# Kernel tuning notes

Hardware: AMD Instinct MI355X
Metric: run time of the kernel (lower is better)

## Reference

```python
import jax, jax.numpy as jnp
import numpy as np

N_FEATURES = 256
HIDDEN_DIM = 256
NUM_HEADS = 8
HEAD_DIM = HIDDEN_DIM // NUM_HEADS
SCALE = HEAD_DIM ** -0.5
H = W = 64


def setup_inputs() -> dict:
    key = jax.random.key(0)
    k1, k2, kq, kk, kv, kp, kb = jax.random.split(key, 7)
    s = 1.0 / np.sqrt(N_FEATURES)
    return {
        "x1": jax.random.normal(k1, (1, N_FEATURES, H, W), dtype=jnp.float32),
        "x2": jax.random.normal(k2, (1, N_FEATURES, H, W), dtype=jnp.float32),
        # 1x1 conv weights reduce to [out_ch, in_ch] matrices
        "Wq": jax.random.uniform(kq, (HIDDEN_DIM, N_FEATURES), jnp.float32, -s, s),
        "Wk": jax.random.uniform(kk, (HIDDEN_DIM, N_FEATURES), jnp.float32, -s, s),
        "Wv": jax.random.uniform(kv, (HIDDEN_DIM, N_FEATURES), jnp.float32, -s, s),
        "Wp": jax.random.uniform(kp, (N_FEATURES, HIDDEN_DIM), jnp.float32, -s, s),
        "bp": jax.random.uniform(kb, (N_FEATURES,), jnp.float32, -s, s),
    }


def reference(x1, x2, Wq, Wk, Wv, Wp, bp):
    B, C, Hh, Ww = x1.shape
    N = Hh * Ww
    # 1x1 convs == channel matmuls; reshape to [B, heads, head_dim, N]
    q = jnp.einsum('oc,bchw->bohw', Wq, x1).reshape(B, NUM_HEADS, HEAD_DIM, N)
    k = jnp.einsum('oc,bchw->bohw', Wk, x2).reshape(B, NUM_HEADS, HEAD_DIM, N)
    v = jnp.einsum('oc,bchw->bohw', Wv, x2).reshape(B, NUM_HEADS, HEAD_DIM, N)
    attn = jnp.einsum('bhcn,bhcm->bhnm', q, k) * SCALE
    attn = jax.nn.softmax(attn, axis=-1)
    fused = jnp.einsum('bhnm,bhcm->bhcn', attn, v)
    fused = fused.reshape(B, HIDDEN_DIM, Hh, Ww)  # requires hidden_dim == C
    out = jnp.einsum('oc,bchw->bohw', Wp, fused) + bp[None, :, None, None]
    return out
```

## Files before the change

### kernel.cpp

```cpp
#include <hip/hip_runtime.h>

#define NPOS 4096
#define NCH  256
#define HD   32
#define KB   128
#define NSPLIT 4
#define SPLIT_KEYS (NPOS / NSPLIT)
#define NSTEP (SPLIT_KEYS / KB)

#define TOFF(o, c) (((((o) >> 4) * 8 + ((c) >> 5)) * 64 + \
                     ((((c) >> 3) & 3) * 16) + ((o) & 15)) * 8 + ((c) & 7))

typedef float f32x4  __attribute__((ext_vector_type(4)));
typedef float f32x16 __attribute__((ext_vector_type(16)));
typedef short s16x8  __attribute__((ext_vector_type(8)));
typedef uint  u32x2  __attribute__((ext_vector_type(2)));
typedef uint  u32x4  __attribute__((ext_vector_type(4)));
typedef int   i32x2  __attribute__((ext_vector_type(2)));

static __device__ __forceinline__ s16x8 load8(const ushort* p) {
    return *(const s16x8*)p;
}
static __device__ __forceinline__ ushort bfbits(float x) {
    __bf16 b = (__bf16)x;
    return __builtin_bit_cast(unsigned short, b);
}
static __device__ __forceinline__ float bfval(ushort u) {
    uint x = (uint)u << 16;
    return __builtin_bit_cast(float, x);
}
static __device__ __forceinline__ uint pk2(float a, float b) {
    return (uint)bfbits(a) | ((uint)bfbits(b) << 16);
}
static __device__ __forceinline__ void plswap(uint& a, uint& b) {
    i32x2 r = __builtin_amdgcn_permlane32_swap((int)a, (int)b, false, false);
    a = (uint)r[0];
    b = (uint)r[1];
}

__global__ __launch_bounds__(256) void convert_kernel(
    const float* __restrict__ x1, const float* __restrict__ x2,
    const float* __restrict__ Wq, const float* __restrict__ Wk,
    const float* __restrict__ Wv, const float* __restrict__ Wp,
    ushort* __restrict__ xt1h, ushort* __restrict__ xt1l,
    ushort* __restrict__ xt2h, ushort* __restrict__ xt2l,
    ushort* __restrict__ wsp, float qscale)
{
    if (blockIdx.z == 2) {
        const int m = blockIdx.y;
        const float* src = m == 0 ? Wq : m == 1 ? Wk : m == 2 ? Wv : Wp;
        const float sc = m == 0 ? qscale : 1.f;
        const int idx = (blockIdx.x * 256 + threadIdx.x) * 4;
        const int o = idx >> 8, c0 = idx & 255;
        f32x4 w = *(const f32x4*)(src + idx);
        w *= sc;
        ushort h[4], l[4];
#pragma unroll
        for (int i = 0; i < 4; ++i) {
            h[i] = bfbits(w[i]);
            l[i] = bfbits(w[i] - bfval(h[i]));
        }
        ushort* H = wsp + m * 2 * 65536;
        const int off = TOFF(o, c0);
        *(u32x2*)(H + off)         = (u32x2){(uint)h[0] | ((uint)h[1] << 16),
                                             (uint)h[2] | ((uint)h[3] << 16)};
        *(u32x2*)(H + 65536 + off) = (u32x2){(uint)l[0] | ((uint)l[1] << 16),
                                             (uint)l[2] | ((uint)l[3] << 16)};
        return;
    }
    __shared__ float tile[64][65];
    const float* X = blockIdx.z ? x2 : x1;
    ushort* Hd = blockIdx.z ? xt2h : xt1h;
    ushort* Ld = blockIdx.z ? xt2l : xt1l;
    const int n0 = blockIdx.x * 64, c0 = blockIdx.y * 64;
    const int tj = threadIdx.x & 63, ti = threadIdx.x >> 6;
#pragma unroll
    for (int r = 0; r < 16; ++r) {
        int i = r * 4 + ti;
        tile[i][tj] = X[(c0 + i) * NPOS + n0 + tj];
    }
    __syncthreads();
#pragma unroll
    for (int r = 0; r < 16; ++r) {
        int i = r * 4 + ti;
        float v = tile[tj][i];
        ushort h = bfbits(v);
        ushort l = bfbits(v - bfval(h));
        const int off = TOFF(n0 + i, c0 + tj);
        Hd[off] = h;
        Ld[off] = l;
    }
}

__global__ __launch_bounds__(256) void gemm_qkv_kernel(
    const ushort* __restrict__ wsp,
    const ushort* __restrict__ x1h, const ushort* __restrict__ x1l,
    const ushort* __restrict__ x2h, const ushort* __restrict__ x2l,
    ushort* __restrict__ qt, ushort* __restrict__ kt, ushort* __restrict__ vt)
{
    const int m  = blockIdx.y >> 2;
    const int ob = blockIdx.y & 3;
    const ushort* Wh = wsp + m * 131072;
    const ushort* Wl = Wh + 65536;
    const ushort* Bh = (m == 0) ? x1h : x2h;
    const ushort* Bl = (m == 0) ? x1l : x2l;

    const int wid = threadIdx.x >> 6, lane = threadIdx.x & 63;
    const int lq = lane & 15, grp = lane >> 4;
    const int o0 = ob * 64 + wid * 16;
    const int n0 = blockIdx.x * 32;
    const int To = o0 >> 4;
    const int Tn = n0 >> 4;

    f32x4 acc[2];
    acc[0] = (f32x4){0.f, 0.f, 0.f, 0.f};
    acc[1] = acc[0];
#pragma unroll
    for (int kc = 0; kc < 8; ++kc) {
        const s16x8 ah = load8(Wh + ((To * 8 + kc) * 64 + lane) * 8);
        const s16x8 al = load8(Wl + ((To * 8 + kc) * 64 + lane) * 8);
#pragma unroll
        for (int nt = 0; nt < 2; ++nt) {
            const s16x8 bh = load8(Bh + (((Tn + nt) * 8 + kc) * 64 + lane) * 8);
            const s16x8 bl = load8(Bl + (((Tn + nt) * 8 + kc) * 64 + lane) * 8);
            acc[nt] = __builtin_amdgcn_mfma_f32_16x16x32_bf16(ah, bh, acc[nt], 0, 0, 0);
            acc[nt] = __builtin_amdgcn_mfma_f32_16x16x32_bf16(ah, bl, acc[nt], 0, 0, 0);
            acc[nt] = __builtin_amdgcn_mfma_f32_16x16x32_bf16(al, bh, acc[nt], 0, 0, 0);
        }
    }
    if (m < 2) {
        ushort* Y = m ? kt : qt;
        const int head = o0 >> 5, d0 = (o0 & 31) + grp * 4;
#pragma unroll
        for (int nt = 0; nt < 2; ++nt) {
            const int n = n0 + nt * 16 + lq;
            *(u32x2*)(Y + head * (NPOS * HD) + n * HD + d0) =
                (u32x2){pk2(acc[nt][0], acc[nt][1]), pk2(acc[nt][2], acc[nt][3])};
        }
    } else {
#pragma unroll
        for (int nt = 0; nt < 2; ++nt) {
            const int n = n0 + nt * 16 + lq;
#pragma unroll
            for (int r = 0; r < 4; ++r)
                vt[(o0 + grp * 4 + r) * NPOS + n] = bfbits(acc[nt][r]);
        }
    }
}

__global__ __launch_bounds__(256) void attn_mfma_kernel(
    const ushort* __restrict__ Qt,
    const ushort* __restrict__ Kt,
    const ushort* __restrict__ Vt,
    ushort* __restrict__ Opb,
    float* __restrict__ Ml)
{
    __shared__ __align__(16) ushort lds[18944];
    const int bid  = blockIdx.x;
    const int s    = bid >> 8;
    const int h    = bid & 7;
    const int qblk = (bid & 255) >> 3;
    const int tid  = threadIdx.x;
    const int wid  = tid >> 6;
    const int lane = tid & 63;
    const int l31  = lane & 31;
    const int hi   = lane >> 5;
    const int q0   = qblk * 128 + wid * 32;
    const int k0   = s * SPLIT_KEYS;
    const int hq   = h * (NPOS * HD);

    s16x8 qf[2];
#pragma unroll
    for (int kh = 0; kh < 2; ++kh)
        qf[kh] = load8(Qt + hq + (q0 + l31) * HD + kh * 16 + hi * 8);

    const int kr0 = tid >> 2, kc0 = tid & 3;
    const ushort* kS = Kt + hq + kr0 * HD + kc0 * 8;
    const int kdst0 = kr0 * 40 + ((kc0 ^ ((kr0 >> 3) & 3)) & 3) * 8;
    const int kdst1 = kdst0 + 64 * 40;

    const int vr0 = tid >> 4, vc0 = tid & 15;
    const ushort* vS = Vt + h * (HD * NPOS) + vr0 * NPOS + vc0 * 8;
    const int vdst0 = vr0 * 136 + ((vc0 ^ ((vr0 >> 3) & 3)) & 15) * 8;
    const int vdst1 = (vr0 + 16) * 136 +
                      ((vc0 ^ (((vr0 + 16) >> 3) & 3)) & 15) * 8;

    const int kx = l31 >> 3;

    f32x16 oacc = {};
    float lacc = 0.f;

    *(s16x8*)(lds + kdst0)         = load8(kS + (size_t)k0 * HD);
    *(s16x8*)(lds + kdst1)         = load8(kS + (size_t)k0 * HD + 64 * HD);
    *(s16x8*)(lds + 10240 + vdst0) = load8(vS + k0);
    *(s16x8*)(lds + 10240 + vdst1) = load8(vS + k0 + 16 * NPOS);
    const int m1 = (NSTEP > 1) ? k0 + KB : k0;
    s16x8 kra = load8(kS + (size_t)m1 * HD);
    s16x8 krb = load8(kS + (size_t)m1 * HD + 64 * HD);
    s16x8 vra = load8(vS + m1);
    s16x8 vrb = load8(vS + m1 + 16 * NPOS);
    __syncthreads();

    for (int step = 0; step < NSTEP; ++step) {
        const int cur = step & 1;
        ushort* const Kb = lds + cur * 5120;
        ushort* const Vb = lds + 10240 + cur * 4352;

        {
            ushort* const Kn = lds + (cur ^ 1) * 5120;
            ushort* const Vn = lds + 10240 + (cur ^ 1) * 4352;
            *(s16x8*)(Kn + kdst0) = kra;
            *(s16x8*)(Kn + kdst1) = krb;
            *(s16x8*)(Vn + vdst0) = vra;
            *(s16x8*)(Vn + vdst1) = vrb;
        }
        const int mn = (step + 2 < NSTEP) ? k0 + (step + 2) * KB : k0;
        kra = load8(kS + (size_t)mn * HD);
        krb = load8(kS + (size_t)mn * HD + 64 * HD);
        vra = load8(vS + mn);
        vrb = load8(vS + mn + 16 * NPOS);

#pragma unroll
        for (int t = 0; t < 4; ++t) {
            const int krow = (t * 32 + l31) * 40;
            const s16x8 kfa = *(const s16x8*)(Kb + krow + ((hi ^ kx) & 3) * 8);
            const s16x8 kfb = *(const s16x8*)(Kb + krow + (((2 + hi) ^ kx) & 3) * 8);
            f32x16 st = {};
            __builtin_amdgcn_s_setprio(1);
            st = __builtin_amdgcn_mfma_f32_32x32x16_bf16(kfa, qf[0], st, 0, 0, 0);
            st = __builtin_amdgcn_mfma_f32_32x32x16_bf16(kfb, qf[1], st, 0, 0, 0);
            __builtin_amdgcn_s_setprio(0);

            const s16x8 vf0 = *(const s16x8*)(Vb + l31 * 136 +
                                              (((t * 4 + hi) ^ kx) & 15) * 8);
            const s16x8 vf1 = *(const s16x8*)(Vb + l31 * 136 +
                                              (((t * 4 + 2 + hi) ^ kx) & 15) * 8);

            uint w[4], w2[4];
            float ls = 0.f;
#pragma unroll
            for (int g = 0; g < 4; ++g) {
                const float p0 = __builtin_amdgcn_exp2f(st[4 * g + 0]);
                const float p1 = __builtin_amdgcn_exp2f(st[4 * g + 1]);
                const float p2 = __builtin_amdgcn_exp2f(st[4 * g + 2]);
                const float p3 = __builtin_amdgcn_exp2f(st[4 * g + 3]);
                ls += (p0 + p1) + (p2 + p3);
                w[g]  = pk2(p0, p1);
                w2[g] = pk2(p2, p3);
            }
            lacc += ls;
            uint a0 = w[0],  c0 = w[1];  plswap(a0, c0);
            uint a1 = w2[0], c1 = w2[1]; plswap(a1, c1);
            const s16x8 pfA = __builtin_bit_cast(s16x8, (u32x4){a0, a1, c0, c1});
            uint b0 = w[2],  d0 = w[3];  plswap(b0, d0);
            uint b1 = w2[2], d1 = w2[3]; plswap(b1, d1);
            const s16x8 pfB = __builtin_bit_cast(s16x8, (u32x4){b0, b1, d0, d1});

            __builtin_amdgcn_s_setprio(1);
            oacc = __builtin_amdgcn_mfma_f32_32x32x16_bf16(vf0, pfA, oacc, 0, 0, 0);
            oacc = __builtin_amdgcn_mfma_f32_32x32x16_bf16(vf1, pfB, oacc, 0, 0, 0);
            __builtin_amdgcn_s_setprio(0);
        }

        __syncthreads();
    }

    {
        uint a = __builtin_bit_cast(uint, lacc), b = a;
        plswap(a, b);
        lacc = __builtin_bit_cast(float, a) + __builtin_bit_cast(float, b);
    }

    const int n = q0 + l31;
    ushort* Ops = Opb + (size_t)s * (NPOS * NCH) + n * NCH + h * HD;
#pragma unroll
    for (int g = 0; g < 4; ++g) {
        *(u32x2*)(Ops + g * 8 + hi * 4) =
            (u32x2){pk2(oacc[4 * g + 0], oacc[4 * g + 1]),
                    pk2(oacc[4 * g + 2], oacc[4 * g + 3])};
    }
    if (lane < 32)
        Ml[(s * 8 + h) * NPOS + n] = lacc;
}

__global__ __launch_bounds__(256) void combine_kernel(
    const ushort* __restrict__ Opb, const float* __restrict__ Ml,
    ushort* __restrict__ FH, ushort* __restrict__ FL)
{
    const int n = blockIdx.x * 4 + (threadIdx.x >> 6);
    const int c = (threadIdx.x & 63) * 4;
    const int h = c >> 5;
    float l = 0.f;
#pragma unroll
    for (int s = 0; s < NSPLIT; ++s)
        l += Ml[(s * 8 + h) * NPOS + n];
    const float inv = 1.f / l;

    float sum[4] = {0.f, 0.f, 0.f, 0.f};
#pragma unroll
    for (int s = 0; s < NSPLIT; ++s) {
        const u32x2 raw = *(const u32x2*)(Opb + (size_t)s * (NPOS * NCH) +
                                          n * NCH + c);
        sum[0] += bfval((ushort)(raw[0] & 0xFFFF));
        sum[1] += bfval((ushort)(raw[0] >> 16));
        sum[2] += bfval((ushort)(raw[1] & 0xFFFF));
        sum[3] += bfval((ushort)(raw[1] >> 16));
    }
    ushort hb[4], lb[4];
#pragma unroll
    for (int i = 0; i < 4; ++i) {
        float f = sum[i] * inv;
        hb[i] = bfbits(f);
        lb[i] = bfbits(f - bfval(hb[i]));
    }
    const int off = TOFF(n, c);
    *(u32x2*)(FH + off) = (u32x2){(uint)hb[0] | ((uint)hb[1] << 16),
                                  (uint)hb[2] | ((uint)hb[3] << 16)};
    *(u32x2*)(FL + off) = (u32x2){(uint)lb[0] | ((uint)lb[1] << 16),
                                  (uint)lb[2] | ((uint)lb[3] << 16)};
}

__global__ __launch_bounds__(256) void gemm_out_kernel(
    const ushort* __restrict__ Wh, const ushort* __restrict__ Wl,
    const ushort* __restrict__ Bh, const ushort* __restrict__ Bl,
    const float* __restrict__ bias, float* __restrict__ Y)
{
    const int wid = threadIdx.x >> 6, lane = threadIdx.x & 63;
    const int lq = lane & 15, grp = lane >> 4;
    const int o0 = blockIdx.y * 64 + wid * 16;
    const int n0 = blockIdx.x * 32;
    const int To = o0 >> 4;
    const int Tn = n0 >> 4;

    f32x4 acc[2];
    acc[0] = (f32x4){0.f, 0.f, 0.f, 0.f};
    acc[1] = acc[0];
#pragma unroll
    for (int kc = 0; kc < 8; ++kc) {
        const s16x8 ah = load8(Wh + ((To * 8 + kc) * 64 + lane) * 8);
        const s16x8 al = load8(Wl + ((To * 8 + kc) * 64 + lane) * 8);
#pragma unroll
        for (int nt = 0; nt < 2; ++nt) {
            const s16x8 bh = load8(Bh + (((Tn + nt) * 8 + kc) * 64 + lane) * 8);
            const s16x8 bl = load8(Bl + (((Tn + nt) * 8 + kc) * 64 + lane) * 8);
            acc[nt] = __builtin_amdgcn_mfma_f32_16x16x32_bf16(ah, bh, acc[nt], 0, 0, 0);
            acc[nt] = __builtin_amdgcn_mfma_f32_16x16x32_bf16(ah, bl, acc[nt], 0, 0, 0);
            acc[nt] = __builtin_amdgcn_mfma_f32_16x16x32_bf16(al, bh, acc[nt], 0, 0, 0);
        }
    }
    const f32x4 b4 = *(const f32x4*)(bias + o0 + grp * 4);
#pragma unroll
    for (int nt = 0; nt < 2; ++nt) {
        const int n = n0 + nt * 16 + lq;
#pragma unroll
        for (int r = 0; r < 4; ++r)
            Y[(o0 + grp * 4 + r) * NPOS + n] = acc[nt][r] + b4[r];
    }
}

extern "C" void kernel_launch(void* const* d_in, const int* in_sizes, int n_in,
                              void* d_out, int out_size, void* d_ws, size_t ws_size,
                              hipStream_t stream) {
    const float* x1 = (const float*)d_in[0];
    const float* x2 = (const float*)d_in[1];
    const float* Wq = (const float*)d_in[2];
    const float* Wk = (const float*)d_in[3];
    const float* Wv = (const float*)d_in[4];
    const float* Wp = (const float*)d_in[5];
    const float* bp = (const float*)d_in[6];
    float* out = (float*)d_out;

    const size_t MB = 1u << 20;
    char* wsc = (char*)d_ws;
    ushort* xt1h = (ushort*)(wsc + 0 * MB);
    ushort* xt1l = (ushort*)(wsc + 2 * MB);
    ushort* xt2h = (ushort*)(wsc + 4 * MB);
    ushort* xt2l = (ushort*)(wsc + 6 * MB);
    ushort* qt   = (ushort*)(wsc + 8 * MB);
    ushort* kt   = (ushort*)(wsc + 10 * MB);
    ushort* vt   = (ushort*)(wsc + 12 * MB);
    ushort* wsp  = (ushort*)(wsc + 14 * MB);
    float*  Ml   = (float*)(wsc + 15 * MB);
    ushort* Opb  = (ushort*)(wsc + 0 * MB);
    ushort* fth  = (ushort*)(wsc + 8 * MB);
    ushort* ftl  = (ushort*)(wsc + 10 * MB);

    const float qscale = (float)(0.17677669529663687 * 1.4426950408889634);

    convert_kernel<<<dim3(64, 4, 3), 256, 0, stream>>>(
        x1, x2, Wq, Wk, Wv, Wp, xt1h, xt1l, xt2h, xt2l, wsp, qscale);

    gemm_qkv_kernel<<<dim3(128, 12), 256, 0, stream>>>(
        wsp, xt1h, xt1l, xt2h, xt2l, qt, kt, vt);

    attn_mfma_kernel<<<1024, 256, 0, stream>>>(qt, kt, vt, Opb, Ml);

    combine_kernel<<<1024, 256, 0, stream>>>(Opb, Ml, fth, ftl);

    ushort* wph = wsp + 393216;
    ushort* wpl = wsp + 458752;
    gemm_out_kernel<<<dim3(128, 4), 256, 0, stream>>>(
        wph, wpl, fth, ftl, bp, out);
}
```

Before: 75.74 us.

## Fuse input conversion into QKV GEMM and combine into output projection

Splits the weight conversion into its own kernel and folds the x1/x2 transpose and bf16 hi/lo split into the QKV GEMM. Each block now stages its 32-column slice of both inputs in LDS and computes all three projections over 128 output rows. It also merges the split-softmax combine step into the output projection, staging the normalized result in LDS so it is never written to global memory. This removes two kernel launches and the global round trips for the converted activations, at the cost of fewer, heavier blocks (256 blocks each) and more registers per thread.

```diff
diff --git a/kernel.cpp b/kernel.cpp
--- a/kernel.cpp
+++ b/kernel.cpp
@@ -38,114 +38,131 @@
     b = (uint)r[1];
 }
 
-__global__ __launch_bounds__(256) void convert_kernel(
-    const float* __restrict__ x1, const float* __restrict__ x2,
+__global__ __launch_bounds__(256) void convert_w_kernel(
     const float* __restrict__ Wq, const float* __restrict__ Wk,
     const float* __restrict__ Wv, const float* __restrict__ Wp,
-    ushort* __restrict__ xt1h, ushort* __restrict__ xt1l,
-    ushort* __restrict__ xt2h, ushort* __restrict__ xt2l,
     ushort* __restrict__ wsp, float qscale)
 {
-    if (blockIdx.z == 2) {
-        const int m = blockIdx.y;
-        const float* src = m == 0 ? Wq : m == 1 ? Wk : m == 2 ? Wv : Wp;
-        const float sc = m == 0 ? qscale : 1.f;
-        const int idx = (blockIdx.x * 256 + threadIdx.x) * 4;
-        const int o = idx >> 8, c0 = idx & 255;
-        f32x4 w = *(const f32x4*)(src + idx);
-        w *= sc;
-        ushort h[4], l[4];
-#pragma unroll
-        for (int i = 0; i < 4; ++i) {
-            h[i] = bfbits(w[i]);
-            l[i] = bfbits(w[i] - bfval(h[i]));
-        }
-        ushort* H = wsp + m * 2 * 65536;
-        const int off = TOFF(o, c0);
-        *(u32x2*)(H + off)         = (u32x2){(uint)h[0] | ((uint)h[1] << 16),
-                                             (uint)h[2] | ((uint)h[3] << 16)};
-        *(u32x2*)(H + 65536 + off) = (u32x2){(uint)l[0] | ((uint)l[1] << 16),
-                                             (uint)l[2] | ((uint)l[3] << 16)};
-        return;
-    }
-    __shared__ float tile[64][65];
-    const float* X = blockIdx.z ? x2 : x1;
-    ushort* Hd = blockIdx.z ? xt2h : xt1h;
-    ushort* Ld = blockIdx.z ? xt2l : xt1l;
-    const int n0 = blockIdx.x * 64, c0 = blockIdx.y * 64;
-    const int tj = threadIdx.x & 63, ti = threadIdx.x >> 6;
-#pragma unroll
-    for (int r = 0; r < 16; ++r) {
-        int i = r * 4 + ti;
-        tile[i][tj] = X[(c0 + i) * NPOS + n0 + tj];
-    }
-    __syncthreads();
-#pragma unroll
-    for (int r = 0; r < 16; ++r) {
-        int i = r * 4 + ti;
-        float v = tile[tj][i];
-        ushort h = bfbits(v);
-        ushort l = bfbits(v - bfval(h));
-        const int off = TOFF(n0 + i, c0 + tj);
-        Hd[off] = h;
-        Ld[off] = l;
-    }
-}
-
-__global__ __launch_bounds__(256) void gemm_qkv_kernel(
+    const int m = blockIdx.y;
+    const float* src = m == 0 ? Wq : m == 1 ? Wk : m == 2 ? Wv : Wp;
+    const float sc = m == 0 ? qscale : 1.f;
+    const int idx = (blockIdx.x * 256 + threadIdx.x) * 4;
+    const int o = idx >> 8, c0 = idx & 255;
+    f32x4 w = *(const f32x4*)(src + idx);
+    w *= sc;
+    ushort h[4], l[4];
+#pragma unroll
+    for (int i = 0; i < 4; ++i) {
+        h[i] = bfbits(w[i]);
+        l[i] = bfbits(w[i] - bfval(h[i]));
+    }
+    ushort* H = wsp + m * 2 * 65536;
+    const int off = TOFF(o, c0);
+    *(u32x2*)(H + off)         = (u32x2){(uint)h[0] | ((uint)h[1] << 16),
+                                         (uint)h[2] | ((uint)h[3] << 16)};
+    *(u32x2*)(H + 65536 + off) = (u32x2){(uint)l[0] | ((uint)l[1] << 16),
+                                         (uint)l[2] | ((uint)l[3] << 16)};
+}
+
+__global__ __launch_bounds__(256) void fused_qkv_kernel(
+    const float* __restrict__ x1, const float* __restrict__ x2,
     const ushort* __restrict__ wsp,
-    const ushort* __restrict__ x1h, const ushort* __restrict__ x1l,
-    const ushort* __restrict__ x2h, const ushort* __restrict__ x2l,
     ushort* __restrict__ qt, ushort* __restrict__ kt, ushort* __restrict__ vt)
 {
-    const int m  = blockIdx.y >> 2;
-    const int ob = blockIdx.y & 3;
-    const ushort* Wh = wsp + m * 131072;
-    const ushort* Wl = Wh + 65536;
-    const ushort* Bh = (m == 0) ? x1h : x2h;
-    const ushort* Bl = (m == 0) ? x1l : x2l;
-
-    const int wid = threadIdx.x >> 6, lane = threadIdx.x & 63;
+    __shared__ __align__(16) ushort lds[32768];
+    const int tid   = threadIdx.x;
+    const int n0    = blockIdx.x * 32;
+    const int obase = blockIdx.y * 128;
+
+    {
+        const int ln = tid & 7;
+        const int cr = tid >> 3;
+#pragma unroll
+        for (int pass = 0; pass < 16; ++pass) {
+            const int c = (pass & 7) * 32 + cr;
+            const float* X = (pass < 8) ? x1 : x2;
+            const int rbase = (pass < 8) ? 0 : 16384;
+            const f32x4 v = *(const f32x4*)(X + (size_t)c * NPOS + n0 + ln * 4);
+#pragma unroll
+            for (int i = 0; i < 4; ++i) {
+                const int nl = ln * 4 + i;
+                const ushort hb = bfbits(v[i]);
+                const ushort lb = bfbits(v[i] - bfval(hb));
+                const int idx = (((nl >> 4) * 8 + (c >> 5)) * 64 +
+                                 (((c >> 3) & 3) * 16) + (nl & 15)) * 8 + (c & 7);
+                lds[rbase + idx]        = hb;
+                lds[rbase + 8192 + idx] = lb;
+            }
+        }
+    }
+    __syncthreads();
+
+    const int wid = tid >> 6, lane = tid & 63;
     const int lq = lane & 15, grp = lane >> 4;
-    const int o0 = ob * 64 + wid * 16;
-    const int n0 = blockIdx.x * 32;
-    const int To = o0 >> 4;
-    const int Tn = n0 >> 4;
-
-    f32x4 acc[2];
-    acc[0] = (f32x4){0.f, 0.f, 0.f, 0.f};
-    acc[1] = acc[0];
+
+    f32x4 acc[3][2][2];
+#pragma unroll
+    for (int m = 0; m < 3; ++m)
+#pragma unroll
+        for (int ot = 0; ot < 2; ++ot)
+#pragma unroll
+            for (int nt = 0; nt < 2; ++nt)
+                acc[m][ot][nt] = (f32x4){0.f, 0.f, 0.f, 0.f};
+
 #pragma unroll
     for (int kc = 0; kc < 8; ++kc) {
-        const s16x8 ah = load8(Wh + ((To * 8 + kc) * 64 + lane) * 8);
-        const s16x8 al = load8(Wl + ((To * 8 + kc) * 64 + lane) * 8);
-#pragma unroll
-        for (int nt = 0; nt < 2; ++nt) {
-            const s16x8 bh = load8(Bh + (((Tn + nt) * 8 + kc) * 64 + lane) * 8);
-            const s16x8 bl = load8(Bl + (((Tn + nt) * 8 + kc) * 64 + lane) * 8);
-            acc[nt] = __builtin_amdgcn_mfma_f32_16x16x32_bf16(ah, bh, acc[nt], 0, 0, 0);
-            acc[nt] = __builtin_amdgcn_mfma_f32_16x16x32_bf16(ah, bl, acc[nt], 0, 0, 0);
-            acc[nt] = __builtin_amdgcn_mfma_f32_16x16x32_bf16(al, bh, acc[nt], 0, 0, 0);
-        }
-    }
-    if (m < 2) {
-        ushort* Y = m ? kt : qt;
-        const int head = o0 >> 5, d0 = (o0 & 31) + grp * 4;
-#pragma unroll
-        for (int nt = 0; nt < 2; ++nt) {
-            const int n = n0 + nt * 16 + lq;
-            *(u32x2*)(Y + head * (NPOS * HD) + n * HD + d0) =
-                (u32x2){pk2(acc[nt][0], acc[nt][1]), pk2(acc[nt][2], acc[nt][3])};
-        }
-    } else {
-#pragma unroll
-        for (int nt = 0; nt < 2; ++nt) {
-            const int n = n0 + nt * 16 + lq;
-#pragma unroll
-            for (int r = 0; r < 4; ++r)
-                vt[(o0 + grp * 4 + r) * NPOS + n] = bfbits(acc[nt][r]);
-        }
-    }
+#pragma unroll
+        for (int m = 0; m < 3; ++m) {
+            const ushort* W = wsp + m * 131072;
+            const int bb = (m == 0) ? 0 : 16384;
+#pragma unroll
+            for (int ot = 0; ot < 2; ++ot) {
+                const int To = (obase + (wid * 2 + ot) * 16) >> 4;
+                const s16x8 ah = load8(W + ((To * 8 + kc) * 64 + lane) * 8);
+                const s16x8 al = load8(W + 65536 + ((To * 8 + kc) * 64 + lane) * 8);
+#pragma unroll
+                for (int nt = 0; nt < 2; ++nt) {
+                    const s16x8 bh = *(const s16x8*)(lds + bb +
+                                        ((nt * 8 + kc) * 64 + lane) * 8);
+                    const s16x8 bl = *(const s16x8*)(lds + bb + 8192 +
+                                        ((nt * 8 + kc) * 64 + lane) * 8);
+                    acc[m][ot][nt] = __builtin_amdgcn_mfma_f32_16x16x32_bf16(
+                        ah, bh, acc[m][ot][nt], 0, 0, 0);
+                    acc[m][ot][nt] = __builtin_amdgcn_mfma_f32_16x16x32_bf16(
+                        ah, bl, acc[m][ot][nt], 0, 0, 0);
+                    acc[m][ot][nt] = __builtin_amdgcn_mfma_f32_16x16x32_bf16(
+                        al, bh, acc[m][ot][nt], 0, 0, 0);
+                }
+            }
+        }
+    }
+
+#pragma unroll
+    for (int m = 0; m < 3; ++m)
+#pragma unroll
+        for (int ot = 0; ot < 2; ++ot) {
+            const int o0 = obase + (wid * 2 + ot) * 16;
+            if (m < 2) {
+                ushort* Y = m ? kt : qt;
+                const int head = o0 >> 5, d0 = (o0 & 31) + grp * 4;
+#pragma unroll
+                for (int nt = 0; nt < 2; ++nt) {
+                    const int n = n0 + nt * 16 + lq;
+                    *(u32x2*)(Y + head * (NPOS * HD) + n * HD + d0) =
+                        (u32x2){pk2(acc[m][ot][nt][0], acc[m][ot][nt][1]),
+                                pk2(acc[m][ot][nt][2], acc[m][ot][nt][3])};
+                }
+            } else {
+#pragma unroll
+                for (int nt = 0; nt < 2; ++nt) {
+                    const int n = n0 + nt * 16 + lq;
+#pragma unroll
+                    for (int r = 0; r < 4; ++r)
+                        vt[(o0 + grp * 4 + r) * NPOS + n] =
+                            bfbits(acc[2][ot][nt][r]);
+                }
+            }
+        }
 }
 
 __global__ __launch_bounds__(256) void attn_mfma_kernel(
@@ -283,78 +300,81 @@
         Ml[(s * 8 + h) * NPOS + n] = lacc;
 }
 
-__global__ __launch_bounds__(256) void combine_kernel(
+__global__ __launch_bounds__(256) void fused_out_kernel(
     const ushort* __restrict__ Opb, const float* __restrict__ Ml,
-    ushort* __restrict__ FH, ushort* __restrict__ FL)
-{
-    const int n = blockIdx.x * 4 + (threadIdx.x >> 6);
-    const int c = (threadIdx.x & 63) * 4;
-    const int h = c >> 5;
-    float l = 0.f;
-#pragma unroll
-    for (int s = 0; s < NSPLIT; ++s)
-        l += Ml[(s * 8 + h) * NPOS + n];
-    const float inv = 1.f / l;
-
-    float sum[4] = {0.f, 0.f, 0.f, 0.f};
-#pragma unroll
-    for (int s = 0; s < NSPLIT; ++s) {
-        const u32x2 raw = *(const u32x2*)(Opb + (size_t)s * (NPOS * NCH) +
-                                          n * NCH + c);
-        sum[0] += bfval((ushort)(raw[0] & 0xFFFF));
-        sum[1] += bfval((ushort)(raw[0] >> 16));
-        sum[2] += bfval((ushort)(raw[1] & 0xFFFF));
-        sum[3] += bfval((ushort)(raw[1] >> 16));
-    }
-    ushort hb[4], lb[4];
-#pragma unroll
-    for (int i = 0; i < 4; ++i) {
-        float f = sum[i] * inv;
-        hb[i] = bfbits(f);
-        lb[i] = bfbits(f - bfval(hb[i]));
-    }
-    const int off = TOFF(n, c);
-    *(u32x2*)(FH + off) = (u32x2){(uint)hb[0] | ((uint)hb[1] << 16),
-                                  (uint)hb[2] | ((uint)hb[3] << 16)};
-    *(u32x2*)(FL + off) = (u32x2){(uint)lb[0] | ((uint)lb[1] << 16),
-                                  (uint)lb[2] | ((uint)lb[3] << 16)};
-}
-
-__global__ __launch_bounds__(256) void gemm_out_kernel(
     const ushort* __restrict__ Wh, const ushort* __restrict__ Wl,
-    const ushort* __restrict__ Bh, const ushort* __restrict__ Bl,
     const float* __restrict__ bias, float* __restrict__ Y)
 {
-    const int wid = threadIdx.x >> 6, lane = threadIdx.x & 63;
+    __shared__ __align__(16) ushort lds[8192];
+    const int tid = threadIdx.x;
+    const int n0  = blockIdx.x * 16;
+
+    {
+        const int nl = tid >> 4;
+        const int c0 = (tid & 15) * 16;
+        const int n  = n0 + nl;
+        const int h  = c0 >> 5;
+        float l = 0.f;
+#pragma unroll
+        for (int s = 0; s < NSPLIT; ++s)
+            l += Ml[(s * 8 + h) * NPOS + n];
+        const float inv = 1.f / l;
+
+        float f[16];
+#pragma unroll
+        for (int i = 0; i < 16; ++i) f[i] = 0.f;
+#pragma unroll
+        for (int s = 0; s < NSPLIT; ++s) {
+            const s16x8 r0 = load8(Opb + (size_t)s * (NPOS * NCH) + n * NCH + c0);
+            const s16x8 r1 = load8(Opb + (size_t)s * (NPOS * NCH) + n * NCH + c0 + 8);
+#pragma unroll
+            for (int i = 0; i < 8; ++i) {
+                f[i]     += bfval((ushort)r0[i]);
+                f[i + 8] += bfval((ushort)r1[i]);
+            }
+        }
+#pragma unroll
+        for (int i = 0; i < 16; ++i) {
+            const int c = c0 + i;
+            const float v = f[i] * inv;
+            const ushort hb = bfbits(v);
+            const ushort lb = bfbits(v - bfval(hb));
+            const int idx = ((c >> 5) * 64 + (((c >> 3) & 3) * 16) + nl) * 8 + (c & 7);
+            lds[idx]        = hb;
+            lds[4096 + idx] = lb;
+        }
+    }
+    __syncthreads();
+
+    const int wid = tid >> 6, lane = tid & 63;
     const int lq = lane & 15, grp = lane >> 4;
-    const int o0 = blockIdx.y * 64 + wid * 16;
-    const int n0 = blockIdx.x * 32;
-    const int To = o0 >> 4;
-    const int Tn = n0 >> 4;
-
-    f32x4 acc[2];
-    acc[0] = (f32x4){0.f, 0.f, 0.f, 0.f};
-    acc[1] = acc[0];
+
+    f32x4 acc[4];
+#pragma unroll
+    for (int ot = 0; ot < 4; ++ot) acc[ot] = (f32x4){0.f, 0.f, 0.f, 0.f};
+
 #pragma unroll
     for (int kc = 0; kc < 8; ++kc) {
-        const s16x8 ah = load8(Wh + ((To * 8 + kc) * 64 + lane) * 8);
-        const s16x8 al = load8(Wl + ((To * 8 + kc) * 64 + lane) * 8);
-#pragma unroll
-        for (int nt = 0; nt < 2; ++nt) {
-            const s16x8 bh = load8(Bh + (((Tn + nt) * 8 + kc) * 64 + lane) * 8);
-            const s16x8 bl = load8(Bl + (((Tn + nt) * 8 + kc) * 64 + lane) * 8);
-            acc[nt] = __builtin_amdgcn_mfma_f32_16x16x32_bf16(ah, bh, acc[nt], 0, 0, 0);
-            acc[nt] = __builtin_amdgcn_mfma_f32_16x16x32_bf16(ah, bl, acc[nt], 0, 0, 0);
-            acc[nt] = __builtin_amdgcn_mfma_f32_16x16x32_bf16(al, bh, acc[nt], 0, 0, 0);
-        }
-    }
-    const f32x4 b4 = *(const f32x4*)(bias + o0 + grp * 4);
-#pragma unroll
-    for (int nt = 0; nt < 2; ++nt) {
-        const int n = n0 + nt * 16 + lq;
+        const s16x8 bh = *(const s16x8*)(lds + (kc * 64 + lane) * 8);
+        const s16x8 bl = *(const s16x8*)(lds + 4096 + (kc * 64 + lane) * 8);
+#pragma unroll
+        for (int ot = 0; ot < 4; ++ot) {
+            const int To = wid * 4 + ot;
+            const s16x8 ah = load8(Wh + ((To * 8 + kc) * 64 + lane) * 8);
+            const s16x8 al = load8(Wl + ((To * 8 + kc) * 64 + lane) * 8);
+            acc[ot] = __builtin_amdgcn_mfma_f32_16x16x32_bf16(ah, bh, acc[ot], 0, 0, 0);
+            acc[ot] = __builtin_amdgcn_mfma_f32_16x16x32_bf16(ah, bl, acc[ot], 0, 0, 0);
+            acc[ot] = __builtin_amdgcn_mfma_f32_16x16x32_bf16(al, bh, acc[ot], 0, 0, 0);
+        }
+    }
+
+#pragma unroll
+    for (int ot = 0; ot < 4; ++ot) {
+        const int o0 = (wid * 4 + ot) * 16;
+        const f32x4 b4 = *(const f32x4*)(bias + o0 + grp * 4);
 #pragma unroll
         for (int r = 0; r < 4; ++r)
-            Y[(o0 + grp * 4 + r) * NPOS + n] = acc[nt][r] + b4[r];
+            Y[(o0 + grp * 4 + r) * NPOS + n0 + lq] = acc[ot][r] + b4[r];
     }
 }
 
@@ -372,33 +392,24 @@
 
     const size_t MB = 1u << 20;
     char* wsc = (char*)d_ws;
-    ushort* xt1h = (ushort*)(wsc + 0 * MB);
-    ushort* xt1l = (ushort*)(wsc + 2 * MB);
-    ushort* xt2h = (ushort*)(wsc + 4 * MB);
-    ushort* xt2l = (ushort*)(wsc + 6 * MB);
     ushort* qt   = (ushort*)(wsc + 8 * MB);
     ushort* kt   = (ushort*)(wsc + 10 * MB);
     ushort* vt   = (ushort*)(wsc + 12 * MB);
     ushort* wsp  = (ushort*)(wsc + 14 * MB);
     float*  Ml   = (float*)(wsc + 15 * MB);
     ushort* Opb  = (ushort*)(wsc + 0 * MB);
-    ushort* fth  = (ushort*)(wsc + 8 * MB);
-    ushort* ftl  = (ushort*)(wsc + 10 * MB);
 
     const float qscale = (float)(0.17677669529663687 * 1.4426950408889634);
 
-    convert_kernel<<<dim3(64, 4, 3), 256, 0, stream>>>(
-        x1, x2, Wq, Wk, Wv, Wp, xt1h, xt1l, xt2h, xt2l, wsp, qscale);
-
-    gemm_qkv_kernel<<<dim3(128, 12), 256, 0, stream>>>(
-        wsp, xt1h, xt1l, xt2h, xt2l, qt, kt, vt);
+    convert_w_kernel<<<dim3(64, 4), 256, 0, stream>>>(
+        Wq, Wk, Wv, Wp, wsp, qscale);
+
+    fused_qkv_kernel<<<dim3(128, 2), 256, 0, stream>>>(
+        x1, x2, wsp, qt, kt, vt);
 
     attn_mfma_kernel<<<1024, 256, 0, stream>>>(qt, kt, vt, Opb, Ml);
-
-    combine_kernel<<<1024, 256, 0, stream>>>(Opb, Ml, fth, ftl);
 
     ushort* wph = wsp + 393216;
     ushort* wpl = wsp + 458752;
-    gemm_out_kernel<<<dim3(128, 4), 256, 0, stream>>>(
-        wph, wpl, fth, ftl, bp, out);
-}
+    fused_out_kernel<<<256, 256, 0, stream>>>(Opb, Ml, wph, wpl, bp, out);
+}
```

Result: no change. 75.98 us (+0.3%).
